# Kernel tuning notes

Measured on AMD Instinct MI355X. Metric: run time of the kernel, lower is better.

## Reference

```python
import jax, jax.numpy as jnp
import numpy as np

B, D, R, E = 16384, 512, 64, 8

def setup_inputs() -> dict:
    key = jax.random.key(0)
    ks = jax.random.split(key, 8)
    return {
        "x0": jax.random.normal(ks[0], (B, D), jnp.float32),
        "x": jax.random.normal(ks[1], (B, D), jnp.float32),
        "U": jax.random.normal(ks[2], (E, D, R), jnp.float32) * 0.02,
        "V": jax.random.normal(ks[3], (E, R, D), jnp.float32) * 0.02,
        "C": jax.random.normal(ks[4], (E, R, R), jnp.float32) * 0.02,
        "b": jnp.zeros((E, D), jnp.float32),
        "Wg": jax.random.normal(ks[5], (E, D), jnp.float32) * 0.02,
        "bg": jnp.zeros((E,), jnp.float32),
    }

def reference(x0, x, U, V, C, b, Wg, bg):
    # gate: softmax over experts
    g = jax.nn.softmax(x @ Wg.T + bg, axis=1)            # [B, E]
    # per-expert low-rank bilinear transform, batched over experts
    xv = jnp.einsum('bd,erd->ber', x, V)                 # x @ V[e].T
    xvc = jnp.einsum('ber,ers->bes', xv, C)              # xv @ C[e]
    proj = jnp.einsum('bes,eds->bed', xvc, U)            # xvc @ U[e].T
    # gated sum: sum_e g_e * (x0*proj_e + b_e + x)
    gproj = jnp.einsum('be,bed->bd', g, proj)
    out = x0 * gproj + g @ b + x * g.sum(axis=1, keepdims=True)
    return out
```

## Files before the change

kernel.cpp:

```cpp
#include <hip/hip_runtime.h>
#include <math.h>


typedef __bf16 bf16_t;
typedef __attribute__((ext_vector_type(8))) __bf16 bf16x8;
typedef __attribute__((ext_vector_type(4))) float  floatx4;

#define MFMA16 __builtin_amdgcn_mfma_f32_16x16x32_bf16

__device__ __forceinline__ void async16(void* lds, const void* gp) {
  __builtin_amdgcn_global_load_lds(
      (__attribute__((address_space(1))) void*)(gp),
      (__attribute__((address_space(3))) void*)(lds), 16, 0, 0);
}

__global__ __launch_bounds__(256) void prep_kernel(
    const float* __restrict__ U, const float* __restrict__ V, const float* __restrict__ C,
    bf16_t* __restrict__ VCc, bf16_t* __restrict__ Ut) {
  const int b = blockIdx.x, t = threadIdx.x;
  if (b < 64) {
    __shared__ alignas(16) char ldsbuf[32768];
    float* ldsC = (float*)ldsbuf;
    float* ldsV = (float*)(ldsbuf + 16384);
    const int e = b >> 3, db = b & 7;
#pragma unroll
    for (int i = 0; i < 4; ++i) {
      int c = i * 256 + t;
      async16(ldsbuf + c * 16, (const char*)C + (size_t)e * 16384 + c * 16);
    }
#pragma unroll
    for (int i = 0; i < 4; ++i) {
      int c = i * 256 + t, r = c >> 4, cc = c & 15;
      async16(ldsbuf + 16384 + c * 16,
              (const char*)V + (size_t)(e * 64 + r) * 2048 + db * 256 + cc * 16);
    }
    __syncthreads();
    const int s = t & 63, dg = t >> 6;
    float acc16[16];
#pragma unroll
    for (int k = 0; k < 16; ++k) acc16[k] = 0.f;
#pragma unroll 4
    for (int r = 0; r < 64; ++r) {
      float cv = ldsC[r * 64 + s];
      floatx4 v[4];
#pragma unroll
      for (int j = 0; j < 4; ++j) v[j] = *(const floatx4*)(ldsV + r * 64 + dg * 16 + j * 4);
#pragma unroll
      for (int j = 0; j < 4; ++j)
#pragma unroll
        for (int k = 0; k < 4; ++k) acc16[j * 4 + k] = fmaf(v[j][k], cv, acc16[j * 4 + k]);
    }
    bf16_t* dst = VCc + (size_t)(e * 64 + s) * 512 + db * 64 + dg * 16;
    bf16x8 o0, o1;
#pragma unroll
    for (int k = 0; k < 8; ++k) { o0[k] = (bf16_t)acc16[k]; o1[k] = (bf16_t)acc16[8 + k]; }
    *(bf16x8*)dst = o0;
    *(bf16x8*)(dst + 8) = o1;
  } else {
    const int base = (b - 64) * 4096 + t * 16;
    const int d = base >> 9, n0 = base & 511;
    const int e = n0 >> 6, s0 = n0 & 63;
    const float* src = U + ((size_t)e * 512 + d) * 64 + s0;
    bf16x8 o0, o1;
#pragma unroll
    for (int k = 0; k < 8; ++k) { o0[k] = (bf16_t)src[k]; o1[k] = (bf16_t)src[8 + k]; }
    *(bf16x8*)(Ut + base) = o0;
    *(bf16x8*)(Ut + base + 8) = o1;
  }
}

__device__ __forceinline__ void stage_B(char* dst, const char* __restrict__ Bt,
                                        int p, int q, int wave, int t) {
#pragma unroll
  for (int k = 0; k < 4; ++k) {
    int c = k * 512 + t;
    int r = c >> 3, Ls = c & 7, gs = Ls ^ (r & 7);
    async16(dst + (k * 512 + wave * 64) * 16,
            Bt + (size_t)(p * 256 + r) * 1024 + q * 128 + gs * 16);
  }
}

__device__ __forceinline__ void gemm_phase(
    const char* ldsX, char* ldsB, const char* __restrict__ Bt,
    int wr, int wc, int lhi, int llo, int wave, int t, floatx4 acc[2][8]) {
  const int rA0 = wr * 32 + llo, rm = rA0 & 7;
  const char* ap0 = ldsX + rA0 * 1024;
  const char* ap1 = ldsX + (rA0 + 16) * 1024;
  const int rB = wc * 64 + llo, rmB = rB & 7;
#pragma unroll
  for (int p = 0; p < 2; ++p) {
#pragma unroll 1
    for (int q = 0; q < 8; ++q) {
      const int s = p * 8 + q;
      __syncthreads();
      if (p < 1 || q < 7) {
        int np = (q < 7) ? p : p + 1;
        int nq = (q + 1) & 7;
        stage_B(ldsB + ((s + 1) & 1) * 32768, Bt, np, nq, wave, t);
      }
      const char* bbuf = ldsB + (s & 1) * 32768;
#pragma unroll
      for (int kt = 0; kt < 2; ++kt) {
        int ck = (q * 2 + kt) * 4 + lhi;
        int g0 = (ck >> 3) * 128, sq = ck & 7;
        bf16x8 a0 = *(const bf16x8*)(ap0 + g0 + ((sq ^ rm) << 4));
        bf16x8 a1 = *(const bf16x8*)(ap1 + g0 + ((sq ^ rm) << 4));
        int sB = kt * 4 + lhi;
        bf16x8 bfr[4];
#pragma unroll
        for (int j = 0; j < 4; ++j)
          bfr[j] = *(const bf16x8*)(bbuf + (rB + j * 16) * 128 + ((sB ^ rmB) << 4));
#pragma unroll
        for (int j = 0; j < 4; ++j) {
          acc[0][p * 4 + j] = MFMA16(a0, bfr[j], acc[0][p * 4 + j], 0, 0, 0);
          acc[1][p * 4 + j] = MFMA16(a1, bfr[j], acc[1][p * 4 + j], 0, 0, 0);
        }
      }
    }
  }
}

__global__ __launch_bounds__(512, 2) void fused_kernel(
    const float* __restrict__ x0, const float* __restrict__ x,
    const bf16_t* __restrict__ VCc, const bf16_t* __restrict__ Ut,
    const float* __restrict__ Wg, const float* __restrict__ bg,
    const float* __restrict__ bvec, float* __restrict__ out) {
  __shared__ alignas(16) char lds[133120];
  char*  ldsX = lds;
  char*  ldsB = lds + 65536;
  float* ldsG = (float*)(lds + 131072);
  const int t = threadIdx.x;
  const int wave = t >> 6, lane = t & 63;
  const int wr = wave >> 2, wc = wave & 3;
  const int lhi = lane >> 4, llo = lane & 15;
  const int m0 = blockIdx.x * 64;

  {
    const float4* xs = (const float4*)(x + (size_t)m0 * 512);
#pragma unroll
    for (int i = 0; i < 8; ++i) {
      int c = i * 512 + t, r = c >> 6, q = c & 63;
      float4 f0 = xs[r * 128 + q * 2];
      float4 f1 = xs[r * 128 + q * 2 + 1];
      bf16x8 v;
      v[0] = (bf16_t)f0.x; v[1] = (bf16_t)f0.y; v[2] = (bf16_t)f0.z; v[3] = (bf16_t)f0.w;
      v[4] = (bf16_t)f1.x; v[5] = (bf16_t)f1.y; v[6] = (bf16_t)f1.z; v[7] = (bf16_t)f1.w;
      int slot = (q & 7) ^ (r & 7);
      *(bf16x8*)(ldsX + r * 1024 + (q >> 3) * 128 + slot * 16) = v;
    }
  }
  stage_B(ldsB, (const char*)VCc, 0, 0, wave, t);

#pragma unroll 1
  for (int p = 0; p < 8; ++p) {
    const int rl = wave * 8 + p;
    const float4* xr = (const float4*)(x + (size_t)(m0 + rl) * 512 + lane * 8);
    float4 xa = xr[0], xb = xr[1];
    float z[8];
#pragma unroll
    for (int e = 0; e < 8; ++e) {
      const float4* wp = (const float4*)(Wg + (size_t)e * 512 + lane * 8);
      float4 wa = wp[0], wb = wp[1];
      z[e] = xa.x * wa.x + xa.y * wa.y + xa.z * wa.z + xa.w * wa.w +
             xb.x * wb.x + xb.y * wb.y + xb.z * wb.z + xb.w * wb.w;
    }
#pragma unroll
    for (int e = 0; e < 8; ++e)
#pragma unroll
      for (int off = 32; off > 0; off >>= 1) z[e] += __shfl_xor(z[e], off, 64);
    if (lane == 0) {
      float mx = -1e30f, ssum = 0.f;
#pragma unroll
      for (int e = 0; e < 8; ++e) { z[e] += bg[e]; mx = fmaxf(mx, z[e]); }
#pragma unroll
      for (int e = 0; e < 8; ++e) { z[e] = __expf(z[e] - mx); ssum += z[e]; }
      float inv = 1.f / ssum;
      float4 ga = {z[0] * inv, z[1] * inv, z[2] * inv, z[3] * inv};
      float4 gb = {z[4] * inv, z[5] * inv, z[6] * inv, z[7] * inv};
      *(float4*)(ldsG + rl * 8) = ga;
      *(float4*)(ldsG + rl * 8 + 4) = gb;
    }
  }

  floatx4 acc[2][8];
#pragma unroll
  for (int i = 0; i < 2; ++i)
#pragma unroll
    for (int jj = 0; jj < 8; ++jj) acc[i][jj] = (floatx4){0.f, 0.f, 0.f, 0.f};
  gemm_phase(ldsX, ldsB, (const char*)VCc, wr, wc, lhi, llo, wave, t, acc);

  stage_B(ldsB, (const char*)Ut, 0, 0, wave, t);
  __syncthreads();

#pragma unroll
  for (int p = 0; p < 2; ++p) {
    const int e = p * 4 + wc;
#pragma unroll
    for (int i = 0; i < 2; ++i)
#pragma unroll
      for (int r = 0; r < 4; ++r) {
        int ml = wr * 32 + i * 16 + lhi * 4 + r;
        float gv = ldsG[ml * 8 + e];
#pragma unroll
        for (int j = 0; j < 4; ++j) {
          int n = p * 256 + wc * 64 + j * 16 + llo;
          int qc = n >> 3, slot = (qc & 7) ^ (ml & 7);
          *(bf16_t*)(ldsX + ml * 1024 + (qc >> 3) * 128 + slot * 16 + (n & 7) * 2) =
              (bf16_t)(acc[i][p * 4 + j][r] * gv);
        }
      }
  }

#pragma unroll
  for (int i = 0; i < 2; ++i)
#pragma unroll
    for (int jj = 0; jj < 8; ++jj) acc[i][jj] = (floatx4){0.f, 0.f, 0.f, 0.f};
  gemm_phase(ldsX, ldsB, (const char*)Ut, wr, wc, lhi, llo, wave, t, acc);

#pragma unroll
  for (int p = 0; p < 2; ++p) {
    float bb[4][8];
#pragma unroll
    for (int j = 0; j < 4; ++j) {
      int n = p * 256 + wc * 64 + j * 16 + llo;
#pragma unroll
      for (int e = 0; e < 8; ++e) bb[j][e] = bvec[(size_t)e * 512 + n];
    }
#pragma unroll
    for (int i = 0; i < 2; ++i)
#pragma unroll
      for (int r = 0; r < 4; ++r) {
        int ml = wr * 32 + i * 16 + lhi * 4 + r;
        float4 ga = *(const float4*)(ldsG + ml * 8);
        float4 gb = *(const float4*)(ldsG + ml * 8 + 4);
        float g8[8] = {ga.x, ga.y, ga.z, ga.w, gb.x, gb.y, gb.z, gb.w};
        float gsum = ga.x + ga.y + ga.z + ga.w + gb.x + gb.y + gb.z + gb.w;
        size_t mrow = (size_t)(m0 + ml) * 512;
#pragma unroll
        for (int j = 0; j < 4; ++j) {
          int n = p * 256 + wc * 64 + j * 16 + llo;
          float bias = 0.f;
#pragma unroll
          for (int e = 0; e < 8; ++e) bias += g8[e] * bb[j][e];
          size_t idx = mrow + n;
          out[idx] = x0[idx] * acc[i][p * 4 + j][r] + bias + x[idx] * gsum;
        }
      }
  }
}

extern "C" void kernel_launch(void* const* d_in, const int* in_sizes, int n_in,
                              void* d_out, int out_size, void* d_ws, size_t ws_size,
                              hipStream_t stream) {
  const float* x0 = (const float*)d_in[0];
  const float* x  = (const float*)d_in[1];
  const float* U  = (const float*)d_in[2];
  const float* V  = (const float*)d_in[3];
  const float* C  = (const float*)d_in[4];
  const float* bv = (const float*)d_in[5];
  const float* Wg = (const float*)d_in[6];
  const float* bg = (const float*)d_in[7];
  float* out = (float*)d_out;

  char* ws = (char*)d_ws;
  bf16_t* VCc = (bf16_t*)(ws);
  bf16_t* Ut  = (bf16_t*)(ws + 524288);

  prep_kernel<<<128, 256, 0, stream>>>(U, V, C, VCc, Ut);
  fused_kernel<<<256, 512, 0, stream>>>(x0, x, VCc, Ut, Wg, bg, bv, out);
}
```

Measured before the change: 161.1 us.

## Replace double-buffered B staging with 4-deep async ring and LDS-staged epilogue

Both GEMM phases are merged into one 64-step loop. B tiles are streamed through a 4-slot LDS ring with three loads in flight, using explicit vmcnt waits and raw barriers in place of a __syncthreads per double-buffer step, so the second GEMM's loads prefetch across the phase boundary. MFMA sections are raised with s_setprio. The epilogue stages accumulators in LDS so x0/x/out are accessed as coalesced float4 rows instead of strided scalars. This costs extra barriers and LDS traffic in the epilogue and relies on hand-counted vmcnt values being correct.

```diff
diff --git a/kernel.cpp b/kernel.cpp
--- a/kernel.cpp
+++ b/kernel.cpp
@@ -69,54 +69,15 @@
   }
 }
 
-__device__ __forceinline__ void stage_B(char* dst, const char* __restrict__ Bt,
-                                        int p, int q, int wave, int t) {
-#pragma unroll
-  for (int k = 0; k < 4; ++k) {
-    int c = k * 512 + t;
-    int r = c >> 3, Ls = c & 7, gs = Ls ^ (r & 7);
-    async16(dst + (k * 512 + wave * 64) * 16,
-            Bt + (size_t)(p * 256 + r) * 1024 + q * 128 + gs * 16);
-  }
-}
-
-__device__ __forceinline__ void gemm_phase(
-    const char* ldsX, char* ldsB, const char* __restrict__ Bt,
-    int wr, int wc, int lhi, int llo, int wave, int t, floatx4 acc[2][8]) {
-  const int rA0 = wr * 32 + llo, rm = rA0 & 7;
-  const char* ap0 = ldsX + rA0 * 1024;
-  const char* ap1 = ldsX + (rA0 + 16) * 1024;
-  const int rB = wc * 64 + llo, rmB = rB & 7;
-#pragma unroll
-  for (int p = 0; p < 2; ++p) {
-#pragma unroll 1
-    for (int q = 0; q < 8; ++q) {
-      const int s = p * 8 + q;
-      __syncthreads();
-      if (p < 1 || q < 7) {
-        int np = (q < 7) ? p : p + 1;
-        int nq = (q + 1) & 7;
-        stage_B(ldsB + ((s + 1) & 1) * 32768, Bt, np, nq, wave, t);
-      }
-      const char* bbuf = ldsB + (s & 1) * 32768;
-#pragma unroll
-      for (int kt = 0; kt < 2; ++kt) {
-        int ck = (q * 2 + kt) * 4 + lhi;
-        int g0 = (ck >> 3) * 128, sq = ck & 7;
-        bf16x8 a0 = *(const bf16x8*)(ap0 + g0 + ((sq ^ rm) << 4));
-        bf16x8 a1 = *(const bf16x8*)(ap1 + g0 + ((sq ^ rm) << 4));
-        int sB = kt * 4 + lhi;
-        bf16x8 bfr[4];
-#pragma unroll
-        for (int j = 0; j < 4; ++j)
-          bfr[j] = *(const bf16x8*)(bbuf + (rB + j * 16) * 128 + ((sB ^ rmB) << 4));
-#pragma unroll
-        for (int j = 0; j < 4; ++j) {
-          acc[0][p * 4 + j] = MFMA16(a0, bfr[j], acc[0][p * 4 + j], 0, 0, 0);
-          acc[1][p * 4 + j] = MFMA16(a1, bfr[j], acc[1][p * 4 + j], 0, 0, 0);
-        }
-      }
-    }
+__device__ __forceinline__ void stage_q(char* ring, const char* __restrict__ Bt,
+                                        int v, int wave, int t) {
+  char* dst = ring + (v & 3) * 16384;
+  const char* src = Bt + (size_t)((v >> 4) & 1) * 262144 + (v & 15) * 64;
+#pragma unroll
+  for (int i = 0; i < 2; ++i) {
+    int c = i * 512 + t;
+    int r = c >> 2, sp = c & 3, sl = sp ^ ((r & 7) >> 1);
+    async16(dst + (i * 512 + wave * 64) * 16, src + (size_t)r * 1024 + sl * 16);
   }
 }
 
@@ -127,7 +88,7 @@
     const float* __restrict__ bvec, float* __restrict__ out) {
   __shared__ alignas(16) char lds[133120];
   char*  ldsX = lds;
-  char*  ldsB = lds + 65536;
+  char*  ring = lds + 65536;
   float* ldsG = (float*)(lds + 131072);
   const int t = threadIdx.x;
   const int wave = t >> 6, lane = t & 63;
@@ -149,7 +110,9 @@
       *(bf16x8*)(ldsX + r * 1024 + (q >> 3) * 128 + slot * 16) = v;
     }
   }
-  stage_B(ldsB, (const char*)VCc, 0, 0, wave, t);
+  stage_q(ring, (const char*)VCc, 0, wave, t);
+  stage_q(ring, (const char*)VCc, 1, wave, t);
+  stage_q(ring, (const char*)VCc, 2, wave, t);
 
 #pragma unroll 1
   for (int p = 0; p < 8; ++p) {
@@ -181,71 +144,156 @@
       *(float4*)(ldsG + rl * 8 + 4) = gb;
     }
   }
-
+  __syncthreads();
+
+  const int rA0 = wr * 32 + llo, rm = llo & 7;
+  const char* ap0 = ldsX + rA0 * 1024;
+  const char* ap1 = ldsX + (rA0 + 16) * 1024;
+  const int bsw = (lhi ^ ((llo & 7) >> 1)) << 4;
+  const int rBb = wc * 64 + llo;
   floatx4 acc[2][8];
 #pragma unroll
   for (int i = 0; i < 2; ++i)
 #pragma unroll
     for (int jj = 0; jj < 8; ++jj) acc[i][jj] = (floatx4){0.f, 0.f, 0.f, 0.f};
-  gemm_phase(ldsX, ldsB, (const char*)VCc, wr, wc, lhi, llo, wave, t, acc);
-
-  stage_B(ldsB, (const char*)Ut, 0, 0, wave, t);
-  __syncthreads();
-
-#pragma unroll
-  for (int p = 0; p < 2; ++p) {
-    const int e = p * 4 + wc;
-#pragma unroll
-    for (int i = 0; i < 2; ++i)
-#pragma unroll
-      for (int r = 0; r < 4; ++r) {
-        int ml = wr * 32 + i * 16 + lhi * 4 + r;
-        float gv = ldsG[ml * 8 + e];
+
+#pragma unroll 1
+  for (int u = 0; u < 64; ++u) {
+    if (u < 61) {
+      const int v = u + 3;
+      stage_q(ring, (v >> 5) ? (const char*)Ut : (const char*)VCc, v, wave, t);
+      asm volatile("s_waitcnt vmcnt(6)" ::: "memory");
+    } else if (u == 61) {
+      asm volatile("s_waitcnt vmcnt(4)" ::: "memory");
+    } else if (u == 62) {
+      asm volatile("s_waitcnt vmcnt(2)" ::: "memory");
+    } else {
+      asm volatile("s_waitcnt vmcnt(0)" ::: "memory");
+    }
+    asm volatile("s_barrier" ::: "memory");
+
+    const int kk = u & 15;
+    const int g0 = (kk >> 1) * 128, sq = 4 * (kk & 1);
+    bf16x8 a0 = *(const bf16x8*)(ap0 + g0 + (((sq + lhi) ^ rm) << 4));
+    bf16x8 a1 = *(const bf16x8*)(ap1 + g0 + (((sq + lhi) ^ rm) << 4));
+    const char* bq = ring + (u & 3) * 16384;
+    bf16x8 bfr[4];
+#pragma unroll
+    for (int j = 0; j < 4; ++j)
+      bfr[j] = *(const bf16x8*)(bq + (rBb + j * 16) * 64 + bsw);
+
+    __builtin_amdgcn_s_setprio(1);
+    if (u < 32) {
+      if ((u & 16) == 0) {
 #pragma unroll
         for (int j = 0; j < 4; ++j) {
-          int n = p * 256 + wc * 64 + j * 16 + llo;
-          int qc = n >> 3, slot = (qc & 7) ^ (ml & 7);
-          *(bf16_t*)(ldsX + ml * 1024 + (qc >> 3) * 128 + slot * 16 + (n & 7) * 2) =
-              (bf16_t)(acc[i][p * 4 + j][r] * gv);
+          acc[0][j] = MFMA16(a0, bfr[j], acc[0][j], 0, 0, 0);
+          acc[1][j] = MFMA16(a1, bfr[j], acc[1][j], 0, 0, 0);
+        }
+      } else {
+#pragma unroll
+        for (int j = 0; j < 4; ++j) {
+          acc[0][4 + j] = MFMA16(a0, bfr[j], acc[0][4 + j], 0, 0, 0);
+          acc[1][4 + j] = MFMA16(a1, bfr[j], acc[1][4 + j], 0, 0, 0);
         }
       }
-  }
-
-#pragma unroll
-  for (int i = 0; i < 2; ++i)
-#pragma unroll
-    for (int jj = 0; jj < 8; ++jj) acc[i][jj] = (floatx4){0.f, 0.f, 0.f, 0.f};
-  gemm_phase(ldsX, ldsB, (const char*)Ut, wr, wc, lhi, llo, wave, t, acc);
-
-#pragma unroll
-  for (int p = 0; p < 2; ++p) {
-    float bb[4][8];
-#pragma unroll
-    for (int j = 0; j < 4; ++j) {
-      int n = p * 256 + wc * 64 + j * 16 + llo;
-#pragma unroll
-      for (int e = 0; e < 8; ++e) bb[j][e] = bvec[(size_t)e * 512 + n];
-    }
-#pragma unroll
-    for (int i = 0; i < 2; ++i)
-#pragma unroll
-      for (int r = 0; r < 4; ++r) {
-        int ml = wr * 32 + i * 16 + lhi * 4 + r;
-        float4 ga = *(const float4*)(ldsG + ml * 8);
-        float4 gb = *(const float4*)(ldsG + ml * 8 + 4);
-        float g8[8] = {ga.x, ga.y, ga.z, ga.w, gb.x, gb.y, gb.z, gb.w};
-        float gsum = ga.x + ga.y + ga.z + ga.w + gb.x + gb.y + gb.z + gb.w;
-        size_t mrow = (size_t)(m0 + ml) * 512;
+    } else {
+      if ((u & 16) == 0) {
 #pragma unroll
         for (int j = 0; j < 4; ++j) {
-          int n = p * 256 + wc * 64 + j * 16 + llo;
-          float bias = 0.f;
-#pragma unroll
-          for (int e = 0; e < 8; ++e) bias += g8[e] * bb[j][e];
-          size_t idx = mrow + n;
-          out[idx] = x0[idx] * acc[i][p * 4 + j][r] + bias + x[idx] * gsum;
+          acc[0][j] = MFMA16(a0, bfr[j], acc[0][j], 0, 0, 0);
+          acc[1][j] = MFMA16(a1, bfr[j], acc[1][j], 0, 0, 0);
+        }
+      } else {
+#pragma unroll
+        for (int j = 0; j < 4; ++j) {
+          acc[0][4 + j] = MFMA16(a0, bfr[j], acc[0][4 + j], 0, 0, 0);
+          acc[1][4 + j] = MFMA16(a1, bfr[j], acc[1][4 + j], 0, 0, 0);
         }
       }
+    }
+    __builtin_amdgcn_s_setprio(0);
+    asm volatile("s_waitcnt lgkmcnt(0)" ::: "memory");
+    asm volatile("s_barrier" ::: "memory");
+
+    if (u == 31) {
+#pragma unroll
+      for (int p = 0; p < 2; ++p) {
+#pragma unroll
+        for (int i = 0; i < 2; ++i)
+#pragma unroll
+          for (int r = 0; r < 4; ++r) {
+            int ml = wr * 32 + i * 16 + lhi * 4 + r;
+            float gv = ldsG[ml * 8 + p * 4 + wc];
+#pragma unroll
+            for (int j = 0; j < 4; ++j) {
+              int n = p * 256 + wc * 64 + j * 16 + llo;
+              int qc = n >> 3, slot = (qc & 7) ^ (ml & 7);
+              *(bf16_t*)(ldsX + ml * 1024 + (qc >> 3) * 128 + slot * 16 + (n & 7) * 2) =
+                  (bf16_t)(acc[i][p * 4 + j][r] * gv);
+            }
+          }
+      }
+      asm volatile("s_waitcnt lgkmcnt(0)" ::: "memory");
+      asm volatile("s_barrier" ::: "memory");
+#pragma unroll
+      for (int i = 0; i < 2; ++i)
+#pragma unroll
+        for (int jj = 0; jj < 8; ++jj) acc[i][jj] = (floatx4){0.f, 0.f, 0.f, 0.f};
+    }
+  }
+
+  float* ldsF = (float*)ldsX;
+#pragma unroll 1
+  for (int p = 0; p < 2; ++p) {
+    if (p == 0) {
+#pragma unroll
+      for (int i = 0; i < 2; ++i)
+#pragma unroll
+        for (int j = 0; j < 4; ++j)
+#pragma unroll
+          for (int r = 0; r < 4; ++r) {
+            int ml = wr * 32 + i * 16 + lhi * 4 + r;
+            ldsF[ml * 256 + wc * 64 + j * 16 + llo] = acc[i][j][r];
+          }
+    } else {
+#pragma unroll
+      for (int i = 0; i < 2; ++i)
+#pragma unroll
+        for (int j = 0; j < 4; ++j)
+#pragma unroll
+          for (int r = 0; r < 4; ++r) {
+            int ml = wr * 32 + i * 16 + lhi * 4 + r;
+            ldsF[ml * 256 + wc * 64 + j * 16 + llo] = acc[i][4 + j][r];
+          }
+    }
+    __syncthreads();
+    floatx4 bb4[8];
+#pragma unroll
+    for (int e = 0; e < 8; ++e)
+      bb4[e] = *(const floatx4*)(bvec + (size_t)e * 512 + p * 256 + lane * 4);
+#pragma unroll
+    for (int k = 0; k < 8; ++k) {
+      int row = k * 8 + wave;
+      floatx4 v = *(const floatx4*)(ldsF + row * 256 + lane * 4);
+      floatx4 ga = *(const floatx4*)(ldsG + row * 8);
+      floatx4 gb = *(const floatx4*)(ldsG + row * 8 + 4);
+      float g8[8] = {ga[0], ga[1], ga[2], ga[3], gb[0], gb[1], gb[2], gb[3]};
+      float gsum = ga[0] + ga[1] + ga[2] + ga[3] + gb[0] + gb[1] + gb[2] + gb[3];
+      size_t idx = (size_t)(m0 + row) * 512 + p * 256 + lane * 4;
+      floatx4 xv0 = *(const floatx4*)(x0 + idx);
+      floatx4 xv  = *(const floatx4*)(x + idx);
+      floatx4 o;
+#pragma unroll
+      for (int c = 0; c < 4; ++c) {
+        float bias = 0.f;
+#pragma unroll
+        for (int e = 0; e < 8; ++e) bias = fmaf(g8[e], bb4[e][c], bias);
+        o[c] = xv0[c] * v[c] + bias + xv[c] * gsum;
+      }
+      *(floatx4*)(out + idx) = o;
+    }
+    if (p == 0) __syncthreads();
   }
 }
 
```

Measured after the change: 182.7 us. +13.4%, slower.
